# Optimization experiments

Measured on AMD Instinct MI355X. Metric: run time of the kernel, lower is better.

The kernel has to match this reference:

```python
import jax, jax.numpy as jnp
import numpy as np

B, S, D, H = 2, 2048, 1024, 16
DK = D // H  # 64


def setup_inputs() -> dict:
    key = jax.random.key(0)
    ks = jax.random.split(key, 10)
    query = jax.random.normal(ks[0], (B, S, D), dtype=jnp.float32)
    key_t = jax.random.normal(ks[1], (B, S, D), dtype=jnp.float32)
    value = jax.random.normal(ks[2], (B, S, D), dtype=jnp.float32)
    # binary mask [batch, q_size, k_size]: causal lower-triangular, same per batch
    mask = jnp.broadcast_to(jnp.tril(jnp.ones((S, S), dtype=jnp.float32)), (B, S, S))
    sc = 0.02
    Wq = jax.random.normal(ks[3], (D, D), dtype=jnp.float32) * sc
    bq = jnp.zeros((D,), dtype=jnp.float32)
    Wk = jax.random.normal(ks[4], (D, D), dtype=jnp.float32) * sc
    bk = jnp.zeros((D,), dtype=jnp.float32)
    Wv = jax.random.normal(ks[5], (D, D), dtype=jnp.float32) * sc
    bv = jnp.zeros((D,), dtype=jnp.float32)
    return {"query": query, "key": key_t, "value": value, "mask": mask,
            "Wq": Wq, "bq": bq, "Wk": Wk, "bk": bk, "Wv": Wv, "bv": bv}


def reference(query, key, value, mask, Wq, bq, Wk, bk, Wv, bv):
    # ReLU-activated Q/K/V projections (Dense(..., activation='relu'))
    Q = jax.nn.relu(query @ Wq + bq)   # [B, Sq, D]
    K = jax.nn.relu(key @ Wk + bk)     # [B, Sk, D]
    V = jax.nn.relu(value @ Wv + bv)   # [B, Sk, D]
    b, sq, _ = Q.shape
    sk = K.shape[1]
    # split-concat head trick == reshape last dim into (H, DK) heads
    Qh = Q.reshape(b, sq, H, DK)
    Kh = K.reshape(b, sk, H, DK)
    Vh = V.reshape(b, sk, H, DK)
    scores = jnp.einsum('bqhd,bkhd->bhqk', Qh, Kh) / jnp.sqrt(jnp.float32(DK))
    m = mask[:, None, :, :]  # broadcast over heads (mask_expander tiles over h)
    scores = scores * m + (1.0 - m) * (-1e10)
    attn = jax.nn.softmax(scores, axis=-1)  # dropout is a no-op (see notes)
    out = jnp.einsum('bhqk,bkhd->bqhd', attn, Vh).reshape(b, sq, H * DK)
    return out
```

## Files before the change

kernel.cpp:

```cpp
#include <hip/hip_runtime.h>
#include <hip/hip_bf16.h>

#define B_  2
#define S_  2048
#define D_  1024
#define H_  16
#define DK_ 64
#define NR  (B_*S_)
#define QT_ 16
#define CPB 40

typedef __bf16 bf16_t;
typedef __attribute__((ext_vector_type(8)))  __bf16 bf16x8;
typedef __attribute__((ext_vector_type(4)))  float  f32x4;
typedef __attribute__((ext_vector_type(16))) float  f32x16;

#define QSCALE (0.125f * 1.44269504088896340736f)

__device__ inline void gl_lds16(const void* g, void* l) {
  __builtin_amdgcn_global_load_lds(
      (const __attribute__((address_space(1))) void*)g,
      (__attribute__((address_space(3))) void*)l, 16, 0, 0);
}

__device__ inline unsigned pack2(float a, float b) {
  union { bf16_t h[2]; unsigned u; } x;
  x.h[0] = (bf16_t)a; x.h[1] = (bf16_t)b;
  return x.u;
}

__device__ inline bf16x8 frag(const bf16_t* p, int r, int j) {
  return *(const bf16x8*)(p + r * 64 + ((j ^ (r & 7)) * 8));
}

__global__ void cvt_fp32_bf16(const float* __restrict__ xq, const float* __restrict__ xk,
                              const float* __restrict__ xv,
                              bf16_t* __restrict__ yq, bf16_t* __restrict__ yk,
                              bf16_t* __restrict__ yv) {
  const int z = blockIdx.y;
  const float* x = z == 0 ? xq : z == 1 ? xk : xv;
  bf16_t*      y = z == 0 ? yq : z == 1 ? yk : yv;
  size_t i = ((size_t)blockIdx.x * 256 + threadIdx.x) * 8;
  float4 a = *(const float4*)(x + i);
  float4 b = *(const float4*)(x + i + 4);
  union { bf16_t h[8]; uint4 u; } o;
  o.h[0] = (bf16_t)a.x; o.h[1] = (bf16_t)a.y; o.h[2] = (bf16_t)a.z; o.h[3] = (bf16_t)a.w;
  o.h[4] = (bf16_t)b.x; o.h[5] = (bf16_t)b.y; o.h[6] = (bf16_t)b.z; o.h[7] = (bf16_t)b.w;
  *(uint4*)(y + i) = o.u;
}

__global__ void transpose_cvt(const float* __restrict__ wq, const float* __restrict__ wk,
                              const float* __restrict__ wv,
                              bf16_t* __restrict__ oq, bf16_t* __restrict__ ok,
                              bf16_t* __restrict__ ov) {
  const int z = blockIdx.z;
  const float* W = z == 0 ? wq : z == 1 ? wk : wv;
  bf16_t*     WT = z == 0 ? oq : z == 1 ? ok : ov;
  __shared__ float t[32][33];
  int x  = blockIdx.x * 32 + threadIdx.x;
  int y0 = blockIdx.y * 32;
  for (int i = threadIdx.y; i < 32; i += 8)
    t[i][threadIdx.x] = W[(size_t)(y0 + i) * D_ + x];
  __syncthreads();
  int k  = y0 + threadIdx.x;
  int n0 = blockIdx.x * 32;
  for (int i = threadIdx.y; i < 32; i += 8)
    WT[(size_t)(n0 + i) * D_ + k] = (bf16_t)t[threadIdx.x][i];
}

__global__ __launch_bounds__(256, 2) void gemm_qkv(
    const bf16_t* __restrict__ Xq, const bf16_t* __restrict__ Xk, const bf16_t* __restrict__ Xv,
    const bf16_t* __restrict__ Wq, const bf16_t* __restrict__ Wk, const bf16_t* __restrict__ Wv,
    const float* __restrict__ bq, const float* __restrict__ bk, const float* __restrict__ bv,
    bf16_t* __restrict__ Yq, bf16_t* __restrict__ Yk, bf16_t* __restrict__ Yv)
{
  const int z = blockIdx.z;
  const bf16_t* X    = z == 0 ? Xq : z == 1 ? Xk : Xv;
  const bf16_t* WT   = z == 0 ? Wq : z == 1 ? Wk : Wv;
  const float*  bias = z == 0 ? bq : z == 1 ? bk : bv;
  bf16_t*       Y    = z == 0 ? Yq : z == 1 ? Yk : Yv;
  const float scale  = z == 0 ? QSCALE : 1.0f;
  const int transposedV = (z == 2);

  __shared__ bf16_t As[128 * 64];
  __shared__ bf16_t Bs[128 * 64];
  const int m0 = blockIdx.x * 128, n0 = blockIdx.y * 128;
  const int t = threadIdx.x, l = t & 63, w = t >> 6;
  const int wm = (w & 1) * 64, wn = (w >> 1) * 64;
  const int lr = l & 15, lg4 = l >> 4;

  f32x4 acc[4][4] = {};

  for (int k0 = 0; k0 < D_; k0 += 64) {
    #pragma unroll
    for (int i = 0; i < 4; i++) {
      int c = i * 256 + t;
      int row = c >> 3, j0 = c & 7;
      int sc = (j0 ^ (row & 7)) * 8;
      gl_lds16(X  + (size_t)(m0 + row) * D_ + k0 + sc, As + c * 8);
      gl_lds16(WT + (size_t)(n0 + row) * D_ + k0 + sc, Bs + c * 8);
    }
    __syncthreads();

    #pragma unroll
    for (int kk = 0; kk < 2; kk++) {
      const int j = kk * 4 + lg4;
      bf16x8 af[4], bfr[4];
      #pragma unroll
      for (int mf = 0; mf < 4; mf++)
        af[mf] = frag(As, wm + mf * 16 + lr, j);
      #pragma unroll
      for (int nf = 0; nf < 4; nf++)
        bfr[nf] = frag(Bs, wn + nf * 16 + lr, j);
      #pragma unroll
      for (int mf = 0; mf < 4; mf++)
        #pragma unroll
        for (int nf = 0; nf < 4; nf++)
          acc[mf][nf] = __builtin_amdgcn_mfma_f32_16x16x32_bf16(
              af[mf], bfr[nf], acc[mf][nf], 0, 0, 0);
    }
    __syncthreads();
  }

  #pragma unroll
  for (int nf = 0; nf < 4; nf++) {
    int col = n0 + wn + nf * 16 + lr;
    float bvv = bias[col];
    #pragma unroll
    for (int mf = 0; mf < 4; mf++) {
      #pragma unroll
      for (int r = 0; r < 4; r++) {
        int row = m0 + wm + mf * 16 + lg4 * 4 + r;
        float v = fmaxf(acc[mf][nf][r] + bvv, 0.f) * scale;
        if (!transposedV) {
          Y[(size_t)row * D_ + col] = (bf16_t)v;
        } else {
          int bb = row >> 11, s = row & (S_ - 1);
          int hh = col >> 6,  dk = col & (DK_ - 1);
          Y[(((size_t)(bb * H_ + hh)) * DK_ + dk) * S_ + s] = (bf16_t)v;
        }
      }
    }
  }
}

__device__ inline void qkt(const bf16_t* kl, const bf16x8* qf, int lq, int hh,
                           f32x16& s0, f32x16& s1) {
  #pragma unroll
  for (int s = 0; s < 4; s++) {
    bf16x8 k0 = frag(kl, lq, 2 * s + hh);
    bf16x8 k1 = frag(kl, lq + 32, 2 * s + hh);
    s0 = __builtin_amdgcn_mfma_f32_32x32x16_bf16(k0, qf[s], s0, 0, 0, 0);
    s1 = __builtin_amdgcn_mfma_f32_32x32x16_bf16(k1, qf[s], s1, 0, 0, 0);
  }
}

__device__ inline void cmask(f32x16& s0, f32x16& s1, int kb, int q, int hh) {
  #pragma unroll
  for (int r = 0; r < 16; r++) {
    int krow = kb + (r & 3) + 8 * (r >> 2) + 4 * hh;
    if (krow > q)      s0[r] = -1e30f;
    if (krow + 32 > q) s1[r] = -1e30f;
  }
}

__device__ inline void pv_quad(const f32x16& p0, const f32x16& p1,
                               const bf16_t* vl, int lq, int hh,
                               f32x16& o0, f32x16& o1) {
  #pragma unroll
  for (int st = 0; st < 4; st++) {
    const f32x16& ps = (st < 2) ? p0 : p1;
    const int bb = (st & 1) * 8;
    unsigned lo0 = pack2(ps[bb + 0], ps[bb + 1]), lo1 = pack2(ps[bb + 2], ps[bb + 3]);
    unsigned hi0 = pack2(ps[bb + 4], ps[bb + 5]), hi1 = pack2(ps[bb + 6], ps[bb + 7]);
    unsigned sA = hh ? lo0 : hi0, sB = hh ? lo1 : hi1;
    unsigned rA = __shfl_xor(sA, 32, 64), rB = __shfl_xor(sB, 32, 64);
    union { unsigned u[4]; bf16x8 v; } pf;
    pf.u[0] = hh ? rA : lo0;  pf.u[1] = hh ? rB : lo1;
    pf.u[2] = hh ? hi0 : rA;  pf.u[3] = hh ? hi1 : rB;
    bf16x8 v0 = frag(vl, lq, 2 * st + hh);
    bf16x8 v1 = frag(vl, lq + 32, 2 * st + hh);
    o0 = __builtin_amdgcn_mfma_f32_32x32x16_bf16(v0, pf.v, o0, 0, 0, 0);
    o1 = __builtin_amdgcn_mfma_f32_32x32x16_bf16(v1, pf.v, o1, 0, 0, 0);
  }
}

__global__ __launch_bounds__(256, 3) void attn_fwd(
    const bf16_t* __restrict__ Q, const bf16_t* __restrict__ K,
    const bf16_t* __restrict__ VT, bf16_t* __restrict__ PO,
    float* __restrict__ PL)
{
  __shared__ bf16_t lbuf[3][8192];

  const int bx = blockIdx.x;
  const int bh = bx / CPB, r = bx - bh * CPB;
  int qt, ch;
  if (r < 4)       { qt = r;                 ch = 0; }
  else if (r < 12) { qt = 4 + ((r - 4) >> 1);  ch = (r - 4) & 1; }
  else if (r < 24) { qt = 8 + (r - 12) / 3;    ch = (r - 12) % 3; }
  else             { qt = 12 + ((r - 24) >> 2); ch = (r - 24) & 3; }
  const int b = bh >> 4, h = bh & 15;
  const int ntiles = 2 * qt + 2;
  const int kt0 = ch * 8;
  const int nt = min(8, ntiles - kt0);

  const int t = threadIdx.x, w = t >> 6, l = t & 63;
  const int q0 = qt * 128 + w * 32;
  const int lq = l & 31, hh = l >> 5;
  const int qq = q0 + lq;
  const int nfull = 2 * qt + (w >> 1);

  const bf16_t* Qb = Q  + ((size_t)(b * S_ + qq)) * D_ + h * DK_;
  const bf16_t* Kb = K  + ((size_t)b * S_) * D_ + h * DK_;
  const bf16_t* Vb = VT + ((size_t)(b * H_ + h)) * ((size_t)DK_ * S_);

  const int r0 = t >> 3, j0 = t & 7;
  const int jx = (j0 ^ (r0 & 7)) * 8;

  #define STAGE_TILE(bi, kt_) do {                                        \
    const int kb_ = (kt_) << 6;                                           \
    bf16_t* Lb = lbuf[bi];                                                \
    gl_lds16(Kb + (size_t)(kb_ + r0) * D_ + jx,      Lb + t * 8);         \
    gl_lds16(Kb + (size_t)(kb_ + r0 + 32) * D_ + jx, Lb + t * 8 + 2048);  \
    gl_lds16(Vb + (size_t)r0 * S_ + kb_ + jx,        Lb + 4096 + t * 8);  \
    gl_lds16(Vb + (size_t)(r0 + 32) * S_ + kb_ + jx, Lb + 4096 + t * 8 + 2048); \
  } while (0)

  bf16x8 qf[4];
  #pragma unroll
  for (int s = 0; s < 4; s++)
    qf[s] = *(const bf16x8*)(Qb + s * 16 + hh * 8);
  asm volatile("s_waitcnt vmcnt(0)" ::: "memory");
  #pragma unroll
  for (int s = 0; s < 4; s++)
    asm volatile("" : "+v"(qf[s]));

  f32x16 o0 = {}, o1 = {};
  f32x16 lacc = {};

  STAGE_TILE(0, kt0);
  STAGE_TILE(1, kt0 + 1);
  asm volatile("s_waitcnt vmcnt(4)" ::: "memory");
  __syncthreads();

  for (int p = 0; p < nt; ++p) {
    const int kt = kt0 + p;
    const int cur = p - (p / 3) * 3;

    if (p + 2 < nt) {
      const int nb = (p + 2) - ((p + 2) / 3) * 3;
      STAGE_TILE(nb, kt + 2);
    }

    if (kt <= nfull) {
      const bf16_t* kl = lbuf[cur];
      const bf16_t* vl = lbuf[cur] + 4096;

      f32x16 s0 = {}, s1 = {};
      __builtin_amdgcn_s_setprio(1);
      qkt(kl, qf, lq, hh, s0, s1);
      __builtin_amdgcn_s_setprio(0);
      if (kt == nfull) cmask(s0, s1, kt << 6, qq, hh);

      f32x16 p0, p1;
      #pragma unroll
      for (int r2 = 0; r2 < 16; r2++) {
        p0[r2] = exp2f(s0[r2]);
        p1[r2] = exp2f(s1[r2]);
        lacc[r2] += p0[r2] + p1[r2];
      }

      __builtin_amdgcn_s_setprio(1);
      pv_quad(p0, p1, vl, lq, hh, o0, o1);
      __builtin_amdgcn_s_setprio(0);
    }

    if (p + 1 < nt) {
      if (p + 2 < nt) asm volatile("s_waitcnt vmcnt(4)" ::: "memory");
      else            asm volatile("s_waitcnt vmcnt(0)" ::: "memory");
      __syncthreads();
    }
  }
  #undef STAGE_TILE

  float lrun = 0.f;
  #pragma unroll
  for (int r2 = 0; r2 < 16; r2++) lrun += lacc[r2];
  lrun += __shfl_xor(lrun, 32, 64);

  bf16_t* po = PO + (size_t)bx * 8192;
  #pragma unroll
  for (int r2 = 0; r2 < 16; r2++) {
    int dk = (r2 & 3) + 8 * (r2 >> 2) + 4 * hh;
    po[dk * 128 + w * 32 + lq]        = (bf16_t)o0[r2];
    po[(dk + 32) * 128 + w * 32 + lq] = (bf16_t)o1[r2];
  }
  if (hh == 0)
    PL[(size_t)bx * 128 + w * 32 + lq] = lrun;
}

__global__ __launch_bounds__(256, 4) void attn_combine(
    const bf16_t* __restrict__ PO, const float* __restrict__ PL,
    float* __restrict__ out)
{
  const int bx = blockIdx.x;
  const int b = bx >> 8, h = (bx >> 4) & 15, qt = bx & 15;
  const int bh = b * H_ + h;
  int base_r, nc;
  if      (qt < 4)  { base_r = qt;                 nc = 1; }
  else if (qt < 8)  { base_r = 4 + 2 * (qt - 4);   nc = 2; }
  else if (qt < 12) { base_r = 12 + 3 * (qt - 8);  nc = 3; }
  else              { base_r = 24 + 4 * (qt - 12); nc = 4; }
  const int base = bh * CPB + base_r;

  __shared__ float ls[64][132];
  __shared__ float inv[128];

  const int t = threadIdx.x;

  float acc[4][8];
  #pragma unroll
  for (int i = 0; i < 4; i++)
    #pragma unroll
    for (int j = 0; j < 8; j++) acc[i][j] = 0.f;

  for (int c = 0; c < nc; ++c) {
    const bf16_t* po = PO + (size_t)(base + c) * 8192;
    #pragma unroll
    for (int i = 0; i < 4; i++) {
      bf16x8 v = *(const bf16x8*)(po + i * 2048 + t * 8);
      #pragma unroll
      for (int j = 0; j < 8; j++) acc[i][j] += (float)v[j];
    }
  }

  if (t < 128) {
    float s = 0.f;
    for (int c = 0; c < nc; ++c) s += PL[(size_t)(base + c) * 128 + t];
    inv[t] = 1.0f / s;
  }

  #pragma unroll
  for (int i = 0; i < 4; i++)
    #pragma unroll
    for (int j = 0; j < 8; j++)
      ls[(t >> 4) + 16 * i][(t & 15) * 8 + j] = acc[i][j];
  __syncthreads();

  const int q = t >> 1, c0 = (t & 1) * 32;
  const float iv = inv[q];
  float* op = out + ((size_t)(b * S_ + qt * 128 + q)) * D_ + h * DK_ + c0;
  #pragma unroll
  for (int v = 0; v < 8; v++) {
    float4 x = { ls[c0 + 4 * v][q] * iv,     ls[c0 + 4 * v + 1][q] * iv,
                 ls[c0 + 4 * v + 2][q] * iv, ls[c0 + 4 * v + 3][q] * iv };
    *(float4*)(op + 4 * v) = x;
  }
}

extern "C" void kernel_launch(void* const* d_in, const int* in_sizes, int n_in,
                              void* d_out, int out_size, void* d_ws, size_t ws_size,
                              hipStream_t stream) {
  const float* query = (const float*)d_in[0];
  const float* keyi  = (const float*)d_in[1];
  const float* val   = (const float*)d_in[2];
  const float* Wq = (const float*)d_in[4];
  const float* bq = (const float*)d_in[5];
  const float* Wk = (const float*)d_in[6];
  const float* bk = (const float*)d_in[7];
  const float* Wv = (const float*)d_in[8];
  const float* bv = (const float*)d_in[9];
  float* out = (float*)d_out;

  const size_t XB = (size_t)NR * D_;
  const size_t WB = (size_t)D_ * D_;
  bf16_t* ws  = (bf16_t*)d_ws;
  bf16_t* Xq  = ws;
  bf16_t* Xk  = Xq  + XB;
  bf16_t* Xv  = Xk  + XB;
  bf16_t* WTq = Xv  + XB;
  bf16_t* WTk = WTq + WB;
  bf16_t* WTv = WTk + WB;
  bf16_t* Qm  = WTv + WB;
  bf16_t* Km  = Qm  + XB;
  bf16_t* VTm = Km  + XB;
  bf16_t* PO  = ws;
  float*  PL  = (float*)((char*)d_ws + 22u * 1024 * 1024);

  dim3 cgrid(XB / (256 * 8), 3);
  cvt_fp32_bf16<<<cgrid, 256, 0, stream>>>(query, keyi, val, Xq, Xk, Xv);

  dim3 tgrid(D_ / 32, D_ / 32, 3), tblk(32, 8);
  transpose_cvt<<<tgrid, tblk, 0, stream>>>(Wq, Wk, Wv, WTq, WTk, WTv);

  dim3 ggrid(NR / 128, D_ / 128, 3);
  gemm_qkv<<<ggrid, 256, 0, stream>>>(Xq, Xk, Xv, WTq, WTk, WTv,
                                      bq, bk, bv, Qm, Km, VTm);

  attn_fwd<<<dim3(B_ * H_ * CPB), 256, 0, stream>>>(Qm, Km, VTm, PO, PL);
  attn_combine<<<dim3(B_ * H_ * QT_), 256, 0, stream>>>(PO, PL, out);
}
```

Measured before the change: 117.2 us.

## Pair adjacent query tiles per 512-thread block to share K/V staging

Each attention block now runs 8 waves covering two adjacent 128-row query tiles of one head, so each staged K/V tile in LDS serves 256 query rows and each thread issues half as many global-to-LDS loads. The work units are also reordered through lookup tables so the longest causal chunks launch first and heads are interleaved across blocks. The combine kernel is updated for the new slot layout. In exchange, blocks are larger and fewer, and the waves of the lower query tile sit idle on the last causal tiles.

```diff
diff --git a/kernel.cpp b/kernel.cpp
--- a/kernel.cpp
+++ b/kernel.cpp
@@ -8,7 +8,7 @@
 #define DK_ 64
 #define NR  (B_*S_)
 #define QT_ 16
-#define CPB 40
+#define CPP 20
 
 typedef __bf16 bf16_t;
 typedef __attribute__((ext_vector_type(8)))  __bf16 bf16x8;
@@ -32,6 +32,10 @@
 __device__ inline bf16x8 frag(const bf16_t* p, int r, int j) {
   return *(const bf16x8*)(p + r * 64 + ((j ^ (r & 7)) * 8));
 }
+
+__device__ const unsigned char ord_p[CPP] = {7,6,5,4,3,2,7,6,5,4,7,6,1,7,5,3,6,4,2,0};
+__device__ const unsigned char ord_c[CPP] = {0,0,0,0,0,0,1,1,1,1,2,2,0,3,2,1,3,2,1,0};
+__device__ const unsigned char cbase[8]   = {0,1,2,4,6,9,12,16};
 
 __global__ void cvt_fp32_bf16(const float* __restrict__ xq, const float* __restrict__ xk,
                               const float* __restrict__ xv,
@@ -185,7 +189,7 @@
   }
 }
 
-__global__ __launch_bounds__(256, 3) void attn_fwd(
+__global__ __launch_bounds__(512, 6) void attn_fwd(
     const bf16_t* __restrict__ Q, const bf16_t* __restrict__ K,
     const bf16_t* __restrict__ VT, bf16_t* __restrict__ PO,
     float* __restrict__ PL)
@@ -193,22 +197,20 @@
   __shared__ bf16_t lbuf[3][8192];
 
   const int bx = blockIdx.x;
-  const int bh = bx / CPB, r = bx - bh * CPB;
-  int qt, ch;
-  if (r < 4)       { qt = r;                 ch = 0; }
-  else if (r < 12) { qt = 4 + ((r - 4) >> 1);  ch = (r - 4) & 1; }
-  else if (r < 24) { qt = 8 + (r - 12) / 3;    ch = (r - 12) % 3; }
-  else             { qt = 12 + ((r - 24) >> 2); ch = (r - 24) & 3; }
+  const int unit = bx >> 5, bh = bx & 31;
+  const int p_ = ord_p[unit], ch = ord_c[unit];
   const int b = bh >> 4, h = bh & 15;
-  const int ntiles = 2 * qt + 2;
   const int kt0 = ch * 8;
-  const int nt = min(8, ntiles - kt0);
+  const int nt = min(8, (4 * p_ + 4) - kt0);
+  const int slotbase = (bh * CPP + cbase[p_] + ch) * 2;
 
   const int t = threadIdx.x, w = t >> 6, l = t & 63;
-  const int q0 = qt * 128 + w * 32;
+  const int u = w >> 2, w4 = w & 3;
+  const int qt = 2 * p_ + u;
+  const int q0 = qt * 128 + w4 * 32;
   const int lq = l & 31, hh = l >> 5;
   const int qq = q0 + lq;
-  const int nfull = 2 * qt + (w >> 1);
+  const int nfull = 2 * qt + (w4 >> 1);
 
   const bf16_t* Qb = Q  + ((size_t)(b * S_ + qq)) * D_ + h * DK_;
   const bf16_t* Kb = K  + ((size_t)b * S_) * D_ + h * DK_;
@@ -217,13 +219,11 @@
   const int r0 = t >> 3, j0 = t & 7;
   const int jx = (j0 ^ (r0 & 7)) * 8;
 
-  #define STAGE_TILE(bi, kt_) do {                                        \
-    const int kb_ = (kt_) << 6;                                           \
-    bf16_t* Lb = lbuf[bi];                                                \
-    gl_lds16(Kb + (size_t)(kb_ + r0) * D_ + jx,      Lb + t * 8);         \
-    gl_lds16(Kb + (size_t)(kb_ + r0 + 32) * D_ + jx, Lb + t * 8 + 2048);  \
-    gl_lds16(Vb + (size_t)r0 * S_ + kb_ + jx,        Lb + 4096 + t * 8);  \
-    gl_lds16(Vb + (size_t)(r0 + 32) * S_ + kb_ + jx, Lb + 4096 + t * 8 + 2048); \
+  #define STAGE_TILE(bi, kt_) do {                                    \
+    const int kb_ = (kt_) << 6;                                       \
+    bf16_t* Lb = lbuf[bi];                                            \
+    gl_lds16(Kb + (size_t)(kb_ + r0) * D_ + jx, Lb + t * 8);          \
+    gl_lds16(Vb + (size_t)r0 * S_ + kb_ + jx,   Lb + 4096 + t * 8);   \
   } while (0)
 
   bf16x8 qf[4];
@@ -240,7 +240,7 @@
 
   STAGE_TILE(0, kt0);
   STAGE_TILE(1, kt0 + 1);
-  asm volatile("s_waitcnt vmcnt(4)" ::: "memory");
+  asm volatile("s_waitcnt vmcnt(2)" ::: "memory");
   __syncthreads();
 
   for (int p = 0; p < nt; ++p) {
@@ -276,7 +276,7 @@
     }
 
     if (p + 1 < nt) {
-      if (p + 2 < nt) asm volatile("s_waitcnt vmcnt(4)" ::: "memory");
+      if (p + 2 < nt) asm volatile("s_waitcnt vmcnt(2)" ::: "memory");
       else            asm volatile("s_waitcnt vmcnt(0)" ::: "memory");
       __syncthreads();
     }
@@ -288,15 +288,15 @@
   for (int r2 = 0; r2 < 16; r2++) lrun += lacc[r2];
   lrun += __shfl_xor(lrun, 32, 64);
 
-  bf16_t* po = PO + (size_t)bx * 8192;
+  bf16_t* po = PO + (size_t)(slotbase + u) * 8192;
   #pragma unroll
   for (int r2 = 0; r2 < 16; r2++) {
     int dk = (r2 & 3) + 8 * (r2 >> 2) + 4 * hh;
-    po[dk * 128 + w * 32 + lq]        = (bf16_t)o0[r2];
-    po[(dk + 32) * 128 + w * 32 + lq] = (bf16_t)o1[r2];
+    po[dk * 128 + w4 * 32 + lq]        = (bf16_t)o0[r2];
+    po[(dk + 32) * 128 + w4 * 32 + lq] = (bf16_t)o1[r2];
   }
   if (hh == 0)
-    PL[(size_t)bx * 128 + w * 32 + lq] = lrun;
+    PL[(size_t)(slotbase + u) * 128 + w4 * 32 + lq] = lrun;
 }
 
 __global__ __launch_bounds__(256, 4) void attn_combine(
@@ -306,12 +306,9 @@
   const int bx = blockIdx.x;
   const int b = bx >> 8, h = (bx >> 4) & 15, qt = bx & 15;
   const int bh = b * H_ + h;
-  int base_r, nc;
-  if      (qt < 4)  { base_r = qt;                 nc = 1; }
-  else if (qt < 8)  { base_r = 4 + 2 * (qt - 4);   nc = 2; }
-  else if (qt < 12) { base_r = 12 + 3 * (qt - 8);  nc = 3; }
-  else              { base_r = 24 + 4 * (qt - 12); nc = 4; }
-  const int base = bh * CPB + base_r;
+  const int p_ = qt >> 1, u = qt & 1;
+  const int nc = (p_ >> 1) + 1;
+  const int slot0 = (bh * CPP + cbase[p_]) * 2 + u;
 
   __shared__ float ls[64][132];
   __shared__ float inv[128];
@@ -325,7 +322,7 @@
     for (int j = 0; j < 8; j++) acc[i][j] = 0.f;
 
   for (int c = 0; c < nc; ++c) {
-    const bf16_t* po = PO + (size_t)(base + c) * 8192;
+    const bf16_t* po = PO + (size_t)(slot0 + 2 * c) * 8192;
     #pragma unroll
     for (int i = 0; i < 4; i++) {
       bf16x8 v = *(const bf16x8*)(po + i * 2048 + t * 8);
@@ -336,7 +333,7 @@
 
   if (t < 128) {
     float s = 0.f;
-    for (int c = 0; c < nc; ++c) s += PL[(size_t)(base + c) * 128 + t];
+    for (int c = 0; c < nc; ++c) s += PL[(size_t)(slot0 + 2 * c) * 128 + t];
     inv[t] = 1.0f / s;
   }
 
@@ -397,6 +394,6 @@
   gemm_qkv<<<ggrid, 256, 0, stream>>>(Xq, Xk, Xv, WTq, WTk, WTv,
                                       bq, bk, bv, Qm, Km, VTm);
 
-  attn_fwd<<<dim3(B_ * H_ * CPB), 256, 0, stream>>>(Qm, Km, VTm, PO, PL);
+  attn_fwd<<<dim3(32 * CPP), 512, 0, stream>>>(Qm, Km, VTm, PO, PL);
   attn_combine<<<dim3(B_ * H_ * QT_), 256, 0, stream>>>(PO, PL, out);
 }
```

Measured after the change: 260.8 us. 2.23x slower.
